# Kernel optimization log

Hardware: AMD Instinct MI355X
Metric: run time of the kernel (lower is better)

The kernel has to match this reference:

```python
import jax, jax.numpy as jnp
import numpy as np

N, E, D, K = 50000, 800000, 128, 128


def _graph_conv(x, src, dst, w, W_rel, b_rel, W_root, n_nodes):
    # PyG GraphConv (aggr='add'): out = lin_rel(sum_j w_ij * x_j) + lin_root(x)
    msg = w[:, None] * x[src]                              # [E, D]
    agg = jax.ops.segment_sum(msg, dst, num_segments=n_nodes)  # [N, D]
    return agg @ W_rel + b_rel + x @ W_root


def setup_inputs() -> dict:
    key = jax.random.key(0)
    ks = jax.random.split(key, 16)
    sc = 1.0 / np.sqrt(D).astype(np.float32)
    inp = {
        "x": jax.random.normal(ks[0], (N, D), dtype=jnp.float32),
        "edge_index": jax.random.randint(ks[1], (2, E), 0, N, dtype=jnp.int64 if jax.config.jax_enable_x64 else jnp.int32),
        "edge_weight": jax.random.uniform(ks[2], (E,), dtype=jnp.float32),
        # GraphConv layer 1
        "W_rel1": jax.random.normal(ks[3], (D, D), dtype=jnp.float32) * sc,
        "b_rel1": jnp.zeros((D,), dtype=jnp.float32),
        "W_root1": jax.random.normal(ks[4], (D, D), dtype=jnp.float32) * sc,
        # GraphConv layer 2
        "W_rel2": jax.random.normal(ks[5], (D, D), dtype=jnp.float32) * sc,
        "b_rel2": jnp.zeros((D,), dtype=jnp.float32),
        "W_root2": jax.random.normal(ks[6], (D, D), dtype=jnp.float32) * sc,
        # MLP: Linear(D,128) + Identity, then final Linear(128,K)
        "W_m1": jax.random.normal(ks[7], (D, 128), dtype=jnp.float32) * sc,
        "b_m1": jnp.zeros((128,), dtype=jnp.float32),
        "W_out": jax.random.normal(ks[8], (128, K), dtype=jnp.float32) * (1.0 / np.sqrt(128).astype(np.float32)),
        "b_out": jnp.zeros((K,), dtype=jnp.float32),
    }
    return inp


def reference(x, edge_index, edge_weight, W_rel1, b_rel1, W_root1,
              W_rel2, b_rel2, W_root2, W_m1, b_m1, W_out, b_out):
    n_nodes = x.shape[0]
    src, dst = edge_index[0], edge_index[1]

    # Message passing stack with ReLU
    h = jax.nn.relu(_graph_conv(x, src, dst, edge_weight, W_rel1, b_rel1, W_root1, n_nodes))
    h = jax.nn.relu(_graph_conv(h, src, dst, edge_weight, W_rel2, b_rel2, W_root2, n_nodes))

    # MLP -> cluster logits (mlp_act = Identity)
    s = (h @ W_m1 + b_m1) @ W_out + b_out                  # [N, K]
    probs = jax.nn.softmax(s, axis=-1)                     # [N, K]

    # dense_mincut_pool losses (computed edge-wise; A = to_dense_adj(edge_index, w))
    # degree d_i = sum_j A[i, j] = scatter of w over src
    deg = jax.ops.segment_sum(edge_weight, src, num_segments=n_nodes)  # [N]
    # mincut_num = trace(S^T A S) = sum_e w_e * <S[src_e], S[dst_e]>
    mincut_num = jnp.einsum('e,ek,ek->', edge_weight, probs[src], probs[dst])
    # mincut_den = trace(S^T D S) = sum_i d_i * ||S_i||^2
    mincut_den = jnp.sum(deg * jnp.sum(probs * probs, axis=-1))
    mc_loss = -(mincut_num / mincut_den)

    # orthogonality loss: || SS/||SS||_F - I/sqrt(K) ||_F
    ss = probs.T @ probs                                   # [K, K]
    k = probs.shape[1]
    o_loss = jnp.linalg.norm(ss / jnp.linalg.norm(ss) - jnp.eye(k, dtype=ss.dtype) / np.float32(np.sqrt(k)))

    return probs, mc_loss, o_loss
```

## Files before the change

kernel.cpp:

```cpp
#include <hip/hip_runtime.h>
#include <hip/hip_bf16.h>

#define D 128
#define KT 32
#define SS_BLOCKS 256

__global__ __launch_bounds__(256) void hist_deg_kernel(const int* __restrict__ src,
                                                       const int* __restrict__ dst,
                                                       const float* __restrict__ w,
                                                       int* __restrict__ cnt,
                                                       float* __restrict__ deg, int E) {
    int e = blockIdx.x * 256 + threadIdx.x;
    if (e < E) {
        atomicAdd(&cnt[dst[e]], 1);
        atomicAdd(&deg[src[e]], w[e]);
    }
}

__global__ __launch_bounds__(256) void scan_chunk_kernel(const int* __restrict__ cnt,
                                                         int* __restrict__ rowptr,
                                                         int* __restrict__ aux, int N) {
    __shared__ int ts[256];
    int t = threadIdx.x;
    int base = blockIdx.x * 1024 + t * 4;
    int v[4], s = 0;
#pragma unroll
    for (int i = 0; i < 4; ++i) {
        v[i] = (base + i < N) ? cnt[base + i] : 0;
        s += v[i];
    }
    ts[t] = s;
    __syncthreads();
#pragma unroll
    for (int off = 1; off < 256; off <<= 1) {
        int add = (t >= off) ? ts[t - off] : 0;
        __syncthreads();
        ts[t] += add;
        __syncthreads();
    }
    int run = ts[t] - s;
#pragma unroll
    for (int i = 0; i < 4; ++i) {
        run += v[i];
        if (base + i < N) rowptr[base + i + 1] = run;
    }
    if (t == 255) aux[blockIdx.x] = ts[255];
}

__global__ void scan_aux_kernel(int* __restrict__ aux, int nb) {
    if (threadIdx.x == 0) {
        int s = 0;
        for (int i = 0; i < nb; ++i) { s += aux[i]; aux[i] = s; }
    }
}

__global__ __launch_bounds__(256) void add_off_kernel(int* __restrict__ rowptr,
                                                      const int* __restrict__ aux, int N) {
    int i = blockIdx.x * 256 + threadIdx.x;
    if (i == 0) rowptr[0] = 0;
    if (i < N) {
        int b = i >> 10;
        if (b > 0) rowptr[i + 1] += aux[b - 1];
    }
}

__global__ __launch_bounds__(256) void fill_kernel(const int* __restrict__ src,
                                                   const int* __restrict__ dst,
                                                   const float* __restrict__ w,
                                                   const int* __restrict__ rowptr,
                                                   int* __restrict__ cur,
                                                   int* __restrict__ csr_src,
                                                   float* __restrict__ csr_w, int E) {
    int e = blockIdx.x * 256 + threadIdx.x;
    if (e < E) {
        int d = dst[e];
        int pos = rowptr[d] + atomicAdd(&cur[d], 1);
        csr_src[pos] = src[e];
        csr_w[pos] = w[e];
    }
}

#define ACC4(acc, we, v) { acc.x += (we) * (v).x; acc.y += (we) * (v).y; \
                           acc.z += (we) * (v).z; acc.w += (we) * (v).w; }

__global__ __launch_bounds__(256) void gather_kernel(const float* __restrict__ xin,
                                                     const int* __restrict__ csr_src,
                                                     const float* __restrict__ csr_w,
                                                     const int* __restrict__ rowptr,
                                                     float* __restrict__ agg, int N) {
    int node = blockIdx.x * 4 + (threadIdx.x >> 6);
    if (node >= N) return;
    int lane = threadIdx.x & 63;
    int half = lane >> 5;
    int c4 = (lane & 31) * 4;
    int beg = rowptr[node], end = rowptr[node + 1];
    float4 a0 = make_float4(0.f, 0.f, 0.f, 0.f);
    float4 a1 = make_float4(0.f, 0.f, 0.f, 0.f);
    int j = beg;
    for (; j + 3 < end; j += 4) {
        int e0 = j + half, e1 = j + 2 + half;
        int s0 = csr_src[e0]; float w0 = csr_w[e0];
        int s1 = csr_src[e1]; float w1 = csr_w[e1];
        float4 v0 = *(const float4*)&xin[(size_t)s0 * D + c4];
        float4 v1 = *(const float4*)&xin[(size_t)s1 * D + c4];
        ACC4(a0, w0, v0);
        ACC4(a1, w1, v1);
    }
    if (j + 1 < end) {
        int e0 = j + half;
        int s0 = csr_src[e0]; float w0 = csr_w[e0];
        float4 v0 = *(const float4*)&xin[(size_t)s0 * D + c4];
        ACC4(a0, w0, v0);
        j += 2;
    }
    if (j < end && half == 0) {
        int s0 = csr_src[j]; float w0 = csr_w[j];
        float4 v0 = *(const float4*)&xin[(size_t)s0 * D + c4];
        ACC4(a0, w0, v0);
    }
    a0.x += a1.x; a0.y += a1.y; a0.z += a1.z; a0.w += a1.w;
    a0.x += __shfl_xor(a0.x, 32);
    a0.y += __shfl_xor(a0.y, 32);
    a0.z += __shfl_xor(a0.z, 32);
    a0.w += __shfl_xor(a0.w, 32);
    if (half == 0) *(float4*)&agg[(size_t)node * D + c4] = a0;
}

#define FMA4(acc, a, wv) { acc.x += (a) * (wv).x; acc.y += (a) * (wv).y; \
                           acc.z += (a) * (wv).z; acc.w += (a) * (wv).w; }

__global__ __launch_bounds__(256) void lin_kernel(const float* __restrict__ A1,
                                                  const float* __restrict__ A2,
                                                  const float* __restrict__ W1,
                                                  const float* __restrict__ W2,
                                                  const float* __restrict__ b,
                                                  float* __restrict__ out, int N) {
    __shared__ float As[KT][132];
    __shared__ float Ws[KT][D];
    int tid = threadIdx.x;
    int r0 = blockIdx.x * 128;
    int ty4 = (tid >> 3) * 4;
    int tx16 = (tid & 7) * 16;

    float4 acc[4][4];
#pragma unroll
    for (int i = 0; i < 4; ++i)
#pragma unroll
        for (int j = 0; j < 4; ++j) acc[i][j] = make_float4(0.f, 0.f, 0.f, 0.f);

    for (int t = 0; t < 8; ++t) {
        const float* A = (t < 4) ? A1 : A2;
        const float* W = (t < 4) ? W1 : W2;
        int koff = (t & 3) * KT;
        __syncthreads();
#pragma unroll
        for (int i = 0; i < 4; ++i) {
            int f4 = tid + i * 256;
            int row = f4 >> 3;
            int c4 = f4 & 7;
            float4 v = make_float4(0.f, 0.f, 0.f, 0.f);
            if (r0 + row < N) v = *(const float4*)&A[(size_t)(r0 + row) * D + koff + c4 * 4];
            As[c4 * 4 + 0][row] = v.x;
            As[c4 * 4 + 1][row] = v.y;
            As[c4 * 4 + 2][row] = v.z;
            As[c4 * 4 + 3][row] = v.w;
        }
#pragma unroll
        for (int i = 0; i < 4; ++i) {
            int f4 = tid + i * 256;
            int k = f4 >> 5;
            int c4 = f4 & 31;
            *(float4*)&Ws[k][c4 * 4] = *(const float4*)&W[(size_t)(koff + k) * D + c4 * 4];
        }
        __syncthreads();
#pragma unroll 4
        for (int k = 0; k < KT; ++k) {
            float4 av = *(const float4*)&As[k][ty4];
            float4 w0 = *(const float4*)&Ws[k][tx16];
            float4 w1 = *(const float4*)&Ws[k][tx16 + 4];
            float4 w2 = *(const float4*)&Ws[k][tx16 + 8];
            float4 w3 = *(const float4*)&Ws[k][tx16 + 12];
            FMA4(acc[0][0], av.x, w0); FMA4(acc[0][1], av.x, w1);
            FMA4(acc[0][2], av.x, w2); FMA4(acc[0][3], av.x, w3);
            FMA4(acc[1][0], av.y, w0); FMA4(acc[1][1], av.y, w1);
            FMA4(acc[1][2], av.y, w2); FMA4(acc[1][3], av.y, w3);
            FMA4(acc[2][0], av.z, w0); FMA4(acc[2][1], av.z, w1);
            FMA4(acc[2][2], av.z, w2); FMA4(acc[2][3], av.z, w3);
            FMA4(acc[3][0], av.w, w0); FMA4(acc[3][1], av.w, w1);
            FMA4(acc[3][2], av.w, w2); FMA4(acc[3][3], av.w, w3);
        }
    }
    float4 bv[4];
#pragma unroll
    for (int j = 0; j < 4; ++j) bv[j] = *(const float4*)&b[tx16 + j * 4];
#pragma unroll
    for (int i = 0; i < 4; ++i) {
        int r = r0 + ty4 + i;
        if (r < N) {
#pragma unroll
            for (int j = 0; j < 4; ++j) {
                float4 v;
                v.x = fmaxf(acc[i][j].x + bv[j].x, 0.f);
                v.y = fmaxf(acc[i][j].y + bv[j].y, 0.f);
                v.z = fmaxf(acc[i][j].z + bv[j].z, 0.f);
                v.w = fmaxf(acc[i][j].w + bv[j].w, 0.f);
                *(float4*)&out[(size_t)r * D + tx16 + j * 4] = v;
            }
        }
    }
}

__global__ __launch_bounds__(256) void smallmm_kernel(const float* __restrict__ Wm1,
                                                      const float* __restrict__ bm1,
                                                      const float* __restrict__ Wout,
                                                      const float* __restrict__ bout,
                                                      float* __restrict__ Wc,
                                                      float* __restrict__ bc) {
    int idx = blockIdx.x * 256 + threadIdx.x;
    if (blockIdx.x < 64) {
        int i = idx >> 7, j = idx & 127;
        float s = 0.f;
        for (int k = 0; k < 128; ++k) s += Wm1[i * 128 + k] * Wout[k * 128 + j];
        Wc[idx] = s;
    } else {
        int j = threadIdx.x;
        if (j < 128) {
            float s = bout[j];
            for (int k = 0; k < 128; ++k) s += bm1[k] * Wout[k * 128 + j];
            bc[j] = s;
        }
    }
}

__global__ __launch_bounds__(256) void out_softmax_kernel(const float* __restrict__ h2,
                                                          const float* __restrict__ Wc,
                                                          const float* __restrict__ bc,
                                                          const float* __restrict__ deg,
                                                          float* __restrict__ probs,
                                                          float* __restrict__ accum, int N) {
    __shared__ float Rs[32][128];
    __shared__ float Ws[128 * 64];
    int tid = threadIdx.x;
    int wave = tid >> 6, lane = tid & 63;
    int r0 = blockIdx.x * 32;
#pragma unroll
    for (int i = 0; i < 4; ++i) {
        int f4 = tid + i * 256;
        int row = f4 >> 5;
        int c4 = f4 & 31;
        float4 v = make_float4(0.f, 0.f, 0.f, 0.f);
        if (r0 + row < N) v = *(const float4*)&h2[(size_t)(r0 + row) * D + c4 * 4];
        *(float4*)&Rs[row][c4 * 4] = v;
    }
    float lg[8][2];
#pragma unroll
    for (int h = 0; h < 2; ++h) {
        __syncthreads();
#pragma unroll
        for (int i = 0; i < 8; ++i) {
            int f4 = tid + i * 256;
            int k = f4 >> 4;
            int c4 = f4 & 15;
            *(float4*)&Ws[k * 64 + c4 * 4] = *(const float4*)&Wc[(size_t)k * 128 + h * 64 + c4 * 4];
        }
        __syncthreads();
        float bv = bc[h * 64 + lane];
        float a[8];
#pragma unroll
        for (int ri = 0; ri < 8; ++ri) a[ri] = bv;
        for (int k = 0; k < 128; ++k) {
            float wv = Ws[k * 64 + lane];
#pragma unroll
            for (int ri = 0; ri < 8; ++ri) a[ri] += Rs[wave + ri * 4][k] * wv;
        }
#pragma unroll
        for (int ri = 0; ri < 8; ++ri) lg[ri][h] = a[ri];
    }
    float den_local = 0.f;
#pragma unroll
    for (int ri = 0; ri < 8; ++ri) {
        int row = wave + ri * 4;
        int gr = r0 + row;
        float m = fmaxf(lg[ri][0], lg[ri][1]);
#pragma unroll
        for (int s = 32; s >= 1; s >>= 1) m = fmaxf(m, __shfl_xor(m, s));
        float e0 = expf(lg[ri][0] - m);
        float e1 = expf(lg[ri][1] - m);
        float sum = e0 + e1;
#pragma unroll
        for (int s = 32; s >= 1; s >>= 1) sum += __shfl_xor(sum, s);
        float inv = 1.f / sum;
        float p0 = e0 * inv, p1 = e1 * inv;
        float sq = p0 * p0 + p1 * p1;
#pragma unroll
        for (int s = 32; s >= 1; s >>= 1) sq += __shfl_xor(sq, s);
        if (gr < N) {
            probs[(size_t)gr * D + lane]      = p0;
            probs[(size_t)gr * D + 64 + lane] = p1;
            if (lane == 0) den_local += deg[gr] * sq;
        }
    }
    if (lane == 0 && den_local != 0.f) atomicAdd(&accum[1], den_local);
}

__global__ __launch_bounds__(256) void num_csr_kernel(const float* __restrict__ probs,
                                                      const int* __restrict__ csr_src,
                                                      const float* __restrict__ csr_w,
                                                      const int* __restrict__ rowptr,
                                                      float* __restrict__ accum, int N) {
    int tid = threadIdx.x;
    int wave = tid >> 6, lane = tid & 63;
    int half = lane >> 5;
    int c4 = (lane & 31) * 4;
    float acc = 0.f;
    int stride = gridDim.x * 4;
    for (int node = blockIdx.x * 4 + wave; node < N; node += stride) {
        float4 pd = *(const float4*)&probs[(size_t)node * D + c4];
        int beg = rowptr[node], end = rowptr[node + 1];
        int j = beg;
        for (; j + 3 < end; j += 4) {
            int e0 = j + half, e1 = j + 2 + half;
            int s0 = csr_src[e0]; float w0 = csr_w[e0];
            int s1 = csr_src[e1]; float w1 = csr_w[e1];
            float4 p0 = *(const float4*)&probs[(size_t)s0 * D + c4];
            float4 p1 = *(const float4*)&probs[(size_t)s1 * D + c4];
            acc += w0 * (p0.x * pd.x + p0.y * pd.y + p0.z * pd.z + p0.w * pd.w)
                 + w1 * (p1.x * pd.x + p1.y * pd.y + p1.z * pd.z + p1.w * pd.w);
        }
        if (j + 1 < end) {
            int e0 = j + half;
            int s0 = csr_src[e0]; float w0 = csr_w[e0];
            float4 p0 = *(const float4*)&probs[(size_t)s0 * D + c4];
            acc += w0 * (p0.x * pd.x + p0.y * pd.y + p0.z * pd.z + p0.w * pd.w);
            j += 2;
        }
        if (j < end && half == 0) {
            int s0 = csr_src[j]; float w0 = csr_w[j];
            float4 p0 = *(const float4*)&probs[(size_t)s0 * D + c4];
            acc += w0 * (p0.x * pd.x + p0.y * pd.y + p0.z * pd.z + p0.w * pd.w);
        }
    }
#pragma unroll
    for (int m = 32; m >= 1; m >>= 1) acc += __shfl_xor(acc, m);
    if (lane == 0 && acc != 0.f) atomicAdd(&accum[0], acc);
}

__global__ __launch_bounds__(256) void ss_kernel(const float* __restrict__ probs,
                                                 float* __restrict__ partial, int N) {
    __shared__ float Ps[32][132];
    int tid = threadIdx.x;
    int a0 = (tid >> 4) * 8;
    int b0 = (tid & 15) * 8;
    float acc[8][8];
#pragma unroll
    for (int i = 0; i < 8; ++i)
#pragma unroll
        for (int j = 0; j < 8; ++j) acc[i][j] = 0.f;

    int rowsPerBlk = (N + gridDim.x - 1) / gridDim.x;
    int rbeg = blockIdx.x * rowsPerBlk;
    int rend = rbeg + rowsPerBlk;
    if (rend > N) rend = N;

    for (int c = rbeg; c < rend; c += 32) {
        int nr = rend - c;
        if (nr > 32) nr = 32;
        __syncthreads();
        for (int i = tid; i < nr * 32; i += 256) {
            int r = i >> 5, c4 = i & 31;
            *(float4*)&Ps[r][c4 * 4] = *(const float4*)&probs[(size_t)(c + r) * D + c4 * 4];
        }
        __syncthreads();
        for (int r = 0; r < nr; ++r) {
            float4 av0 = *(const float4*)&Ps[r][a0];
            float4 av1 = *(const float4*)&Ps[r][a0 + 4];
            float4 bv0 = *(const float4*)&Ps[r][b0];
            float4 bv1 = *(const float4*)&Ps[r][b0 + 4];
            float av[8] = {av0.x, av0.y, av0.z, av0.w, av1.x, av1.y, av1.z, av1.w};
            float bv[8] = {bv0.x, bv0.y, bv0.z, bv0.w, bv1.x, bv1.y, bv1.z, bv1.w};
#pragma unroll
            for (int i = 0; i < 8; ++i)
#pragma unroll
                for (int j = 0; j < 8; ++j) acc[i][j] += av[i] * bv[j];
        }
    }
    float* pb = partial + (size_t)blockIdx.x * 16384;
#pragma unroll
    for (int i = 0; i < 8; ++i) {
        *(float4*)&pb[(a0 + i) * 128 + b0]     = make_float4(acc[i][0], acc[i][1], acc[i][2], acc[i][3]);
        *(float4*)&pb[(a0 + i) * 128 + b0 + 4] = make_float4(acc[i][4], acc[i][5], acc[i][6], acc[i][7]);
    }
}

__global__ __launch_bounds__(256) void ss_reduce_kernel(const float* __restrict__ partial,
                                                        float* __restrict__ ss) {
    int i = blockIdx.x * 256 + threadIdx.x;
    float s = 0.f;
    for (int b = 0; b < SS_BLOCKS; ++b) s += partial[(size_t)b * 16384 + i];
    ss[i] = s;
}

__global__ __launch_bounds__(256) void finalize_kernel(const float* __restrict__ ss,
                                                       const float* __restrict__ accum,
                                                       float* __restrict__ out2) {
    int tid = threadIdx.x;
    __shared__ float wsum[4], wsum2[4];
    float s = 0.f;
    for (int i = tid; i < 16384; i += 256) { float v = ss[i]; s += v * v; }
#pragma unroll
    for (int m = 32; m >= 1; m >>= 1) s += __shfl_xor(s, m);
    if ((tid & 63) == 0) wsum[tid >> 6] = s;
    __syncthreads();
    float norm = sqrtf(wsum[0] + wsum[1] + wsum[2] + wsum[3]);
    float inv = 1.f / norm;
    const float rk = 0.08838834764831845f;
    float o = 0.f;
    for (int i = tid; i < 16384; i += 256) {
        int a = i >> 7, b = i & 127;
        float v = ss[i] * inv - (a == b ? rk : 0.f);
        o += v * v;
    }
#pragma unroll
    for (int m = 32; m >= 1; m >>= 1) o += __shfl_xor(o, m);
    if ((tid & 63) == 0) wsum2[tid >> 6] = o;
    __syncthreads();
    if (tid == 0) {
        out2[0] = -(accum[0] / accum[1]);
        out2[1] = sqrtf(wsum2[0] + wsum2[1] + wsum2[2] + wsum2[3]);
    }
}

extern "C" void kernel_launch(void* const* d_in, const int* in_sizes, int n_in,
                              void* d_out, int out_size, void* d_ws, size_t ws_size,
                              hipStream_t stream) {
    const float* x      = (const float*)d_in[0];
    const int*   ei     = (const int*)d_in[1];
    const float* w      = (const float*)d_in[2];
    const float* Wrel1  = (const float*)d_in[3];
    const float* brel1  = (const float*)d_in[4];
    const float* Wroot1 = (const float*)d_in[5];
    const float* Wrel2  = (const float*)d_in[6];
    const float* brel2  = (const float*)d_in[7];
    const float* Wroot2 = (const float*)d_in[8];
    const float* Wm1    = (const float*)d_in[9];
    const float* bm1    = (const float*)d_in[10];
    const float* Wout   = (const float*)d_in[11];
    const float* bout   = (const float*)d_in[12];

    int N = in_sizes[0] / D;
    int E = in_sizes[2];
    const int* src = ei;
    const int* dst = ei + E;

    float* probs = (float*)d_out;
    float* out2  = probs + (size_t)N * D;
    float* h2    = probs;

    float* ws    = (float*)d_ws;
    float* agg   = ws;
    float* h1    = ws + (size_t)N * D;
    float* Wc    = ws + (size_t)2 * N * D;
    float* bc    = Wc + 16384;
    float* ssb   = bc + 128;
    float* deg   = ssb + 16384;
    float* accum = deg + N;
    float* csr_w = accum + 2;
    int*   cnt   = (int*)(csr_w + E);
    int*   cur   = cnt + N;
    int*   rowptr= cur + N;
    int*   aux   = rowptr + N + 1;
    int*   csr_src = aux + 64;

    hipMemsetAsync(deg, 0, (size_t)(N + 2) * sizeof(float), stream);
    hipMemsetAsync(cnt, 0, (size_t)2 * N * sizeof(int), stream);

    int eGrid = (E + 255) / 256;
    int nb = (N + 1023) / 1024;
    int linGrid = (N + 127) / 128;
    int nodeGrid = (N + 3) / 4;

    hist_deg_kernel<<<eGrid, 256, 0, stream>>>(src, dst, w, cnt, deg, E);
    scan_chunk_kernel<<<nb, 256, 0, stream>>>(cnt, rowptr, aux, N);
    scan_aux_kernel<<<1, 64, 0, stream>>>(aux, nb);
    add_off_kernel<<<(N + 255) / 256, 256, 0, stream>>>(rowptr, aux, N);
    fill_kernel<<<eGrid, 256, 0, stream>>>(src, dst, w, rowptr, cur, csr_src, csr_w, E);

    gather_kernel<<<nodeGrid, 256, 0, stream>>>(x, csr_src, csr_w, rowptr, agg, N);
    lin_kernel<<<linGrid, 256, 0, stream>>>(agg, x, Wrel1, Wroot1, brel1, h1, N);
    gather_kernel<<<nodeGrid, 256, 0, stream>>>(h1, csr_src, csr_w, rowptr, agg, N);
    lin_kernel<<<linGrid, 256, 0, stream>>>(agg, h1, Wrel2, Wroot2, brel2, h2, N);
    smallmm_kernel<<<65, 256, 0, stream>>>(Wm1, bm1, Wout, bout, Wc, bc);
    out_softmax_kernel<<<(N + 31) / 32, 256, 0, stream>>>(h2, Wc, bc, deg, probs, accum, N);
    num_csr_kernel<<<2048, 256, 0, stream>>>(probs, csr_src, csr_w, rowptr, accum, N);
    ss_kernel<<<SS_BLOCKS, 256, 0, stream>>>(probs, agg, N);
    ss_reduce_kernel<<<64, 256, 0, stream>>>(agg, ssb);
    finalize_kernel<<<1, 256, 0, stream>>>(ssb, accum, out2);
}
```

Baseline: 728.6 us.

## Store bf16 probs for mincut gather, fuse num and ss kernels, widen gather ILP

The histogram kernel now records each edge's slot from its atomic, so the CSR fill no longer needs a second atomic pass or a cursor array. The feature gather keeps eight independent edge loads in flight per iteration to hide memory latency. Softmax also writes a bf16 copy of probs, which the mincut numerator gather reads to halve its random-access traffic. The numerator and S^T S kernels are merged into one launch so both run concurrently. The bf16 numerator loses some precision relative to fp32.

```diff
diff --git a/kernel.cpp b/kernel.cpp
--- a/kernel.cpp
+++ b/kernel.cpp
@@ -4,15 +4,20 @@
 #define D 128
 #define KT 32
 #define SS_BLOCKS 256
+#define NUM_BLOCKS 2048
+
+__device__ __forceinline__ float bfl(unsigned u) { return __uint_as_float(u << 16); }
+__device__ __forceinline__ float bfh(unsigned u) { return __uint_as_float(u & 0xffff0000u); }
 
 __global__ __launch_bounds__(256) void hist_deg_kernel(const int* __restrict__ src,
                                                        const int* __restrict__ dst,
                                                        const float* __restrict__ w,
                                                        int* __restrict__ cnt,
-                                                       float* __restrict__ deg, int E) {
+                                                       float* __restrict__ deg,
+                                                       int* __restrict__ slot, int E) {
     int e = blockIdx.x * 256 + threadIdx.x;
     if (e < E) {
-        atomicAdd(&cnt[dst[e]], 1);
+        slot[e] = atomicAdd(&cnt[dst[e]], 1);
         atomicAdd(&deg[src[e]], w[e]);
     }
 }
@@ -68,13 +73,12 @@
                                                    const int* __restrict__ dst,
                                                    const float* __restrict__ w,
                                                    const int* __restrict__ rowptr,
-                                                   int* __restrict__ cur,
+                                                   const int* __restrict__ slot,
                                                    int* __restrict__ csr_src,
                                                    float* __restrict__ csr_w, int E) {
     int e = blockIdx.x * 256 + threadIdx.x;
     if (e < E) {
-        int d = dst[e];
-        int pos = rowptr[d] + atomicAdd(&cur[d], 1);
+        int pos = rowptr[dst[e]] + slot[e];
         csr_src[pos] = src[e];
         csr_w[pos] = w[e];
     }
@@ -94,36 +98,53 @@
     int half = lane >> 5;
     int c4 = (lane & 31) * 4;
     int beg = rowptr[node], end = rowptr[node + 1];
-    float4 a0 = make_float4(0.f, 0.f, 0.f, 0.f);
-    float4 a1 = make_float4(0.f, 0.f, 0.f, 0.f);
+    float4 a[8];
+#pragma unroll
+    for (int i = 0; i < 8; ++i) a[i] = make_float4(0.f, 0.f, 0.f, 0.f);
     int j = beg;
-    for (; j + 3 < end; j += 4) {
-        int e0 = j + half, e1 = j + 2 + half;
-        int s0 = csr_src[e0]; float w0 = csr_w[e0];
-        int s1 = csr_src[e1]; float w1 = csr_w[e1];
-        float4 v0 = *(const float4*)&xin[(size_t)s0 * D + c4];
-        float4 v1 = *(const float4*)&xin[(size_t)s1 * D + c4];
-        ACC4(a0, w0, v0);
-        ACC4(a1, w1, v1);
-    }
-    if (j + 1 < end) {
+    for (; j + 15 < end; j += 16) {
+        int ei[8], si[8];
+        float wi[8];
+#pragma unroll
+        for (int i = 0; i < 8; ++i) {
+            ei[i] = j + 2 * i + half;
+            si[i] = csr_src[ei[i]];
+            wi[i] = csr_w[ei[i]];
+        }
+        float4 v[8];
+#pragma unroll
+        for (int i = 0; i < 8; ++i) v[i] = *(const float4*)&xin[(size_t)si[i] * D + c4];
+#pragma unroll
+        for (int i = 0; i < 8; ++i) ACC4(a[i], wi[i], v[i]);
+    }
+    for (; j + 7 < end; j += 8) {
+#pragma unroll
+        for (int i = 0; i < 4; ++i) {
+            int e0 = j + 2 * i + half;
+            int s0 = csr_src[e0]; float w0 = csr_w[e0];
+            float4 v0 = *(const float4*)&xin[(size_t)s0 * D + c4];
+            ACC4(a[i], w0, v0);
+        }
+    }
+    for (; j + 1 < end; j += 2) {
         int e0 = j + half;
         int s0 = csr_src[e0]; float w0 = csr_w[e0];
         float4 v0 = *(const float4*)&xin[(size_t)s0 * D + c4];
-        ACC4(a0, w0, v0);
-        j += 2;
+        ACC4(a[0], w0, v0);
     }
     if (j < end && half == 0) {
         int s0 = csr_src[j]; float w0 = csr_w[j];
         float4 v0 = *(const float4*)&xin[(size_t)s0 * D + c4];
-        ACC4(a0, w0, v0);
-    }
-    a0.x += a1.x; a0.y += a1.y; a0.z += a1.z; a0.w += a1.w;
-    a0.x += __shfl_xor(a0.x, 32);
-    a0.y += __shfl_xor(a0.y, 32);
-    a0.z += __shfl_xor(a0.z, 32);
-    a0.w += __shfl_xor(a0.w, 32);
-    if (half == 0) *(float4*)&agg[(size_t)node * D + c4] = a0;
+        ACC4(a[0], w0, v0);
+    }
+    float4 r = a[0];
+#pragma unroll
+    for (int i = 1; i < 8; ++i) { r.x += a[i].x; r.y += a[i].y; r.z += a[i].z; r.w += a[i].w; }
+    r.x += __shfl_xor(r.x, 32);
+    r.y += __shfl_xor(r.y, 32);
+    r.z += __shfl_xor(r.z, 32);
+    r.w += __shfl_xor(r.w, 32);
+    if (half == 0) *(float4*)&agg[(size_t)node * D + c4] = r;
 }
 
 #define FMA4(acc, a, wv) { acc.x += (a) * (wv).x; acc.y += (a) * (wv).y; \
@@ -237,6 +258,7 @@
                                                           const float* __restrict__ bc,
                                                           const float* __restrict__ deg,
                                                           float* __restrict__ probs,
+                                                          unsigned short* __restrict__ pbh,
                                                           float* __restrict__ accum, int N) {
     __shared__ float Rs[32][128];
     __shared__ float Ws[128 * 64];
@@ -297,99 +319,120 @@
         if (gr < N) {
             probs[(size_t)gr * D + lane]      = p0;
             probs[(size_t)gr * D + 64 + lane] = p1;
+            unsigned u0 = __float_as_uint(p0), u1 = __float_as_uint(p1);
+            pbh[(size_t)gr * D + lane]      = (unsigned short)((u0 + 0x8000u) >> 16);
+            pbh[(size_t)gr * D + 64 + lane] = (unsigned short)((u1 + 0x8000u) >> 16);
             if (lane == 0) den_local += deg[gr] * sq;
         }
     }
     if (lane == 0 && den_local != 0.f) atomicAdd(&accum[1], den_local);
 }
 
-__global__ __launch_bounds__(256) void num_csr_kernel(const float* __restrict__ probs,
-                                                      const int* __restrict__ csr_src,
-                                                      const float* __restrict__ csr_w,
-                                                      const int* __restrict__ rowptr,
-                                                      float* __restrict__ accum, int N) {
+__global__ __launch_bounds__(256) void num_ss_kernel(const float* __restrict__ probs,
+                                                     const unsigned short* __restrict__ pbh,
+                                                     const int* __restrict__ csr_src,
+                                                     const float* __restrict__ csr_w,
+                                                     const int* __restrict__ rowptr,
+                                                     float* __restrict__ accum,
+                                                     float* __restrict__ partial, int N) {
     int tid = threadIdx.x;
+    if (blockIdx.x < SS_BLOCKS) {
+        __shared__ float Ps[32][132];
+        int a0 = (tid >> 4) * 8;
+        int b0 = (tid & 15) * 8;
+        float acc[8][8];
+#pragma unroll
+        for (int i = 0; i < 8; ++i)
+#pragma unroll
+            for (int j = 0; j < 8; ++j) acc[i][j] = 0.f;
+
+        int rowsPerBlk = (N + SS_BLOCKS - 1) / SS_BLOCKS;
+        int rbeg = blockIdx.x * rowsPerBlk;
+        int rend = rbeg + rowsPerBlk;
+        if (rend > N) rend = N;
+
+        for (int c = rbeg; c < rend; c += 32) {
+            int nr = rend - c;
+            if (nr > 32) nr = 32;
+            __syncthreads();
+            for (int i = tid; i < nr * 32; i += 256) {
+                int r = i >> 5, c4 = i & 31;
+                *(float4*)&Ps[r][c4 * 4] = *(const float4*)&probs[(size_t)(c + r) * D + c4 * 4];
+            }
+            __syncthreads();
+            for (int r = 0; r < nr; ++r) {
+                float4 av0 = *(const float4*)&Ps[r][a0];
+                float4 av1 = *(const float4*)&Ps[r][a0 + 4];
+                float4 bv0 = *(const float4*)&Ps[r][b0];
+                float4 bv1 = *(const float4*)&Ps[r][b0 + 4];
+                float av[8] = {av0.x, av0.y, av0.z, av0.w, av1.x, av1.y, av1.z, av1.w};
+                float bv[8] = {bv0.x, bv0.y, bv0.z, bv0.w, bv1.x, bv1.y, bv1.z, bv1.w};
+#pragma unroll
+                for (int i = 0; i < 8; ++i)
+#pragma unroll
+                    for (int j = 0; j < 8; ++j) acc[i][j] += av[i] * bv[j];
+            }
+        }
+        float* pb = partial + (size_t)blockIdx.x * 16384;
+#pragma unroll
+        for (int i = 0; i < 8; ++i) {
+            *(float4*)&pb[(a0 + i) * 128 + b0]     = make_float4(acc[i][0], acc[i][1], acc[i][2], acc[i][3]);
+            *(float4*)&pb[(a0 + i) * 128 + b0 + 4] = make_float4(acc[i][4], acc[i][5], acc[i][6], acc[i][7]);
+        }
+        return;
+    }
+    int bid = blockIdx.x - SS_BLOCKS;
     int wave = tid >> 6, lane = tid & 63;
-    int half = lane >> 5;
-    int c4 = (lane & 31) * 4;
+    int q = lane >> 4;
+    int c8 = (lane & 15) * 8;
     float acc = 0.f;
-    int stride = gridDim.x * 4;
-    for (int node = blockIdx.x * 4 + wave; node < N; node += stride) {
-        float4 pd = *(const float4*)&probs[(size_t)node * D + c4];
+    int stride = NUM_BLOCKS * 4;
+    for (int node = bid * 4 + wave; node < N; node += stride) {
+        float4 pdA = *(const float4*)&probs[(size_t)node * D + c8];
+        float4 pdB = *(const float4*)&probs[(size_t)node * D + c8 + 4];
         int beg = rowptr[node], end = rowptr[node + 1];
         int j = beg;
+        for (; j + 15 < end; j += 16) {
+            int si[4]; float wi[4]; uint4 qv[4];
+#pragma unroll
+            for (int i = 0; i < 4; ++i) {
+                int e = j + 4 * i + q;
+                si[i] = csr_src[e];
+                wi[i] = csr_w[e];
+            }
+#pragma unroll
+            for (int i = 0; i < 4; ++i) qv[i] = *(const uint4*)&pbh[(size_t)si[i] * D + c8];
+#pragma unroll
+            for (int i = 0; i < 4; ++i) {
+                acc += wi[i] * (bfl(qv[i].x) * pdA.x + bfh(qv[i].x) * pdA.y
+                              + bfl(qv[i].y) * pdA.z + bfh(qv[i].y) * pdA.w
+                              + bfl(qv[i].z) * pdB.x + bfh(qv[i].z) * pdB.y
+                              + bfl(qv[i].w) * pdB.z + bfh(qv[i].w) * pdB.w);
+            }
+        }
         for (; j + 3 < end; j += 4) {
-            int e0 = j + half, e1 = j + 2 + half;
-            int s0 = csr_src[e0]; float w0 = csr_w[e0];
-            int s1 = csr_src[e1]; float w1 = csr_w[e1];
-            float4 p0 = *(const float4*)&probs[(size_t)s0 * D + c4];
-            float4 p1 = *(const float4*)&probs[(size_t)s1 * D + c4];
-            acc += w0 * (p0.x * pd.x + p0.y * pd.y + p0.z * pd.z + p0.w * pd.w)
-                 + w1 * (p1.x * pd.x + p1.y * pd.y + p1.z * pd.z + p1.w * pd.w);
-        }
-        if (j + 1 < end) {
-            int e0 = j + half;
-            int s0 = csr_src[e0]; float w0 = csr_w[e0];
-            float4 p0 = *(const float4*)&probs[(size_t)s0 * D + c4];
-            acc += w0 * (p0.x * pd.x + p0.y * pd.y + p0.z * pd.z + p0.w * pd.w);
-            j += 2;
-        }
-        if (j < end && half == 0) {
-            int s0 = csr_src[j]; float w0 = csr_w[j];
-            float4 p0 = *(const float4*)&probs[(size_t)s0 * D + c4];
-            acc += w0 * (p0.x * pd.x + p0.y * pd.y + p0.z * pd.z + p0.w * pd.w);
+            int e = j + q;
+            int s0 = csr_src[e]; float w0 = csr_w[e];
+            uint4 qv = *(const uint4*)&pbh[(size_t)s0 * D + c8];
+            acc += w0 * (bfl(qv.x) * pdA.x + bfh(qv.x) * pdA.y
+                       + bfl(qv.y) * pdA.z + bfh(qv.y) * pdA.w
+                       + bfl(qv.z) * pdB.x + bfh(qv.z) * pdB.y
+                       + bfl(qv.w) * pdB.z + bfh(qv.w) * pdB.w);
+        }
+        int rem = end - j;
+        if (q < rem) {
+            int e = j + q;
+            int s0 = csr_src[e]; float w0 = csr_w[e];
+            uint4 qv = *(const uint4*)&pbh[(size_t)s0 * D + c8];
+            acc += w0 * (bfl(qv.x) * pdA.x + bfh(qv.x) * pdA.y
+                       + bfl(qv.y) * pdA.z + bfh(qv.y) * pdA.w
+                       + bfl(qv.z) * pdB.x + bfh(qv.z) * pdB.y
+                       + bfl(qv.w) * pdB.z + bfh(qv.w) * pdB.w);
         }
     }
 #pragma unroll
     for (int m = 32; m >= 1; m >>= 1) acc += __shfl_xor(acc, m);
     if (lane == 0 && acc != 0.f) atomicAdd(&accum[0], acc);
-}
-
-__global__ __launch_bounds__(256) void ss_kernel(const float* __restrict__ probs,
-                                                 float* __restrict__ partial, int N) {
-    __shared__ float Ps[32][132];
-    int tid = threadIdx.x;
-    int a0 = (tid >> 4) * 8;
-    int b0 = (tid & 15) * 8;
-    float acc[8][8];
-#pragma unroll
-    for (int i = 0; i < 8; ++i)
-#pragma unroll
-        for (int j = 0; j < 8; ++j) acc[i][j] = 0.f;
-
-    int rowsPerBlk = (N + gridDim.x - 1) / gridDim.x;
-    int rbeg = blockIdx.x * rowsPerBlk;
-    int rend = rbeg + rowsPerBlk;
-    if (rend > N) rend = N;
-
-    for (int c = rbeg; c < rend; c += 32) {
-        int nr = rend - c;
-        if (nr > 32) nr = 32;
-        __syncthreads();
-        for (int i = tid; i < nr * 32; i += 256) {
-            int r = i >> 5, c4 = i & 31;
-            *(float4*)&Ps[r][c4 * 4] = *(const float4*)&probs[(size_t)(c + r) * D + c4 * 4];
-        }
-        __syncthreads();
-        for (int r = 0; r < nr; ++r) {
-            float4 av0 = *(const float4*)&Ps[r][a0];
-            float4 av1 = *(const float4*)&Ps[r][a0 + 4];
-            float4 bv0 = *(const float4*)&Ps[r][b0];
-            float4 bv1 = *(const float4*)&Ps[r][b0 + 4];
-            float av[8] = {av0.x, av0.y, av0.z, av0.w, av1.x, av1.y, av1.z, av1.w};
-            float bv[8] = {bv0.x, bv0.y, bv0.z, bv0.w, bv1.x, bv1.y, bv1.z, bv1.w};
-#pragma unroll
-            for (int i = 0; i < 8; ++i)
-#pragma unroll
-                for (int j = 0; j < 8; ++j) acc[i][j] += av[i] * bv[j];
-        }
-    }
-    float* pb = partial + (size_t)blockIdx.x * 16384;
-#pragma unroll
-    for (int i = 0; i < 8; ++i) {
-        *(float4*)&pb[(a0 + i) * 128 + b0]     = make_float4(acc[i][0], acc[i][1], acc[i][2], acc[i][3]);
-        *(float4*)&pb[(a0 + i) * 128 + b0 + 4] = make_float4(acc[i][4], acc[i][5], acc[i][6], acc[i][7]);
-    }
 }
 
 __global__ __launch_bounds__(256) void ss_reduce_kernel(const float* __restrict__ partial,
@@ -466,33 +509,35 @@
     float* accum = deg + N;
     float* csr_w = accum + 2;
     int*   cnt   = (int*)(csr_w + E);
-    int*   cur   = cnt + N;
-    int*   rowptr= cur + N;
+    int*   rowptr= cnt + N;
     int*   aux   = rowptr + N + 1;
     int*   csr_src = aux + 64;
+    int*   slot  = csr_src + E;
+
+    unsigned short* pbh = (unsigned short*)h1;
 
     hipMemsetAsync(deg, 0, (size_t)(N + 2) * sizeof(float), stream);
-    hipMemsetAsync(cnt, 0, (size_t)2 * N * sizeof(int), stream);
+    hipMemsetAsync(cnt, 0, (size_t)N * sizeof(int), stream);
 
     int eGrid = (E + 255) / 256;
     int nb = (N + 1023) / 1024;
     int linGrid = (N + 127) / 128;
     int nodeGrid = (N + 3) / 4;
 
-    hist_deg_kernel<<<eGrid, 256, 0, stream>>>(src, dst, w, cnt, deg, E);
+    hist_deg_kernel<<<eGrid, 256, 0, stream>>>(src, dst, w, cnt, deg, slot, E);
     scan_chunk_kernel<<<nb, 256, 0, stream>>>(cnt, rowptr, aux, N);
     scan_aux_kernel<<<1, 64, 0, stream>>>(aux, nb);
     add_off_kernel<<<(N + 255) / 256, 256, 0, stream>>>(rowptr, aux, N);
-    fill_kernel<<<eGrid, 256, 0, stream>>>(src, dst, w, rowptr, cur, csr_src, csr_w, E);
+    fill_kernel<<<eGrid, 256, 0, stream>>>(src, dst, w, rowptr, slot, csr_src, csr_w, E);
 
     gather_kernel<<<nodeGrid, 256, 0, stream>>>(x, csr_src, csr_w, rowptr, agg, N);
     lin_kernel<<<linGrid, 256, 0, stream>>>(agg, x, Wrel1, Wroot1, brel1, h1, N);
     gather_kernel<<<nodeGrid, 256, 0, stream>>>(h1, csr_src, csr_w, rowptr, agg, N);
     lin_kernel<<<linGrid, 256, 0, stream>>>(agg, h1, Wrel2, Wroot2, brel2, h2, N);
     smallmm_kernel<<<65, 256, 0, stream>>>(Wm1, bm1, Wout, bout, Wc, bc);
-    out_softmax_kernel<<<(N + 31) / 32, 256, 0, stream>>>(h2, Wc, bc, deg, probs, accum, N);
-    num_csr_kernel<<<2048, 256, 0, stream>>>(probs, csr_src, csr_w, rowptr, accum, N);
-    ss_kernel<<<SS_BLOCKS, 256, 0, stream>>>(probs, agg, N);
+    out_softmax_kernel<<<(N + 31) / 32, 256, 0, stream>>>(h2, Wc, bc, deg, probs, pbh, accum, N);
+    num_ss_kernel<<<SS_BLOCKS + NUM_BLOCKS, 256, 0, stream>>>(probs, pbh, csr_src, csr_w,
+                                                              rowptr, accum, agg, N);
     ss_reduce_kernel<<<64, 256, 0, stream>>>(agg, ssb);
     finalize_kernel<<<1, 256, 0, stream>>>(ssb, accum, out2);
 }
```

Result: faster. 638.5 us (-12.4%).
